# Kernel optimization log

Measured on AMD Instinct MI355X. Metric: run time of the kernel, lower is better.

Reference implementation:

```python
import jax, jax.numpy as jnp
import numpy as np
from jax import lax

NSAMPLE = 1024
SEM_NUM = 20


def weighted_fps(xyz, w, nsample):
    # xyz: [B,N,3], w: [B,N] -> idx [B,nsample] int32
    # Iterative weighted furthest point sampling: start at index 0, keep the
    # min squared distance to the selected set, pick argmax(min_dist * weight).
    B, N, _ = xyz.shape
    barange = jnp.arange(B)

    def step(carry, _):
        min_d, last = carry                      # [B,N], [B]
        lp = xyz[barange, last]                  # [B,3] last selected points
        d = jnp.sum((xyz - lp[:, None, :]) ** 2, axis=-1)  # [B,N]
        min_d = jnp.minimum(min_d, d)
        nxt = jnp.argmax(min_d * w, axis=1).astype(jnp.int32)
        return (min_d, nxt), nxt

    init = (jnp.full((B, N), 1e10, xyz.dtype), jnp.zeros((B,), jnp.int32))
    _, rest = lax.scan(step, init, None, length=nsample - 1)   # [nsample-1, B]
    idx = jnp.concatenate([jnp.zeros((1, B), jnp.int32), rest], axis=0)
    return idx.T                                               # [B, nsample]


def setup_inputs() -> dict:
    key = jax.random.key(0)
    k1, k2, k3 = jax.random.split(key, 3)
    B, N, C = 16, 16384, 128
    xyz = jax.random.normal(k1, (B, N, 3), dtype=jnp.float32)
    seg_feature = jax.random.normal(k2, (B, C, N), dtype=jnp.float32)
    seg_label = jax.random.randint(k3, (B, N), 0, SEM_NUM, dtype=jnp.int32)
    return {"xyz": xyz, "seg_feature": seg_feature, "seg_label": seg_label}


def reference(xyz, seg_feature, seg_label):
    # class frequency weights: count[b,c] = #points of class c in cloud b
    counts = jnp.sum(jax.nn.one_hot(seg_label, SEM_NUM, dtype=jnp.float32), axis=1)  # [B,SEM]
    seg_weights = jnp.take_along_axis(counts, seg_label, axis=1)                     # [B,N]
    idx = weighted_fps(lax.stop_gradient(xyz), seg_weights, NSAMPLE)                 # [B,S]
    sampled_xyz = jnp.take_along_axis(xyz, idx[:, :, None], axis=1)                  # [B,S,3]
    sample_seg_feature = jnp.take_along_axis(seg_feature, idx[:, None, :], axis=2)   # [B,C,S]
    sample_seg_label = jnp.take_along_axis(seg_label, idx, axis=1)                   # [B,S]
    return sampled_xyz, sample_seg_feature, sample_seg_label
```

## Files before the change

### kernel.cpp

```cpp
#include <hip/hip_runtime.h>


#define FPS_B   16
#define FPS_N   16384
#define FPS_C   128
#define FPS_S   1024
#define FPS_SEM 20
#define FPS_T   1024
#define FPS_PPT 16

typedef unsigned long long ull;

template <int CTRL>
__device__ __forceinline__ float dpp_movf(float v) {
  return __uint_as_float(__builtin_amdgcn_update_dpp(
      __float_as_uint(v), __float_as_uint(v), CTRL, 0xF, 0xF, true));
}

__global__ __launch_bounds__(FPS_T)
__attribute__((amdgpu_waves_per_eu(4, 4)))
void wfps_kernel(
    const float* __restrict__ xyz,
    const int*   __restrict__ label,
    int*         __restrict__ idx_out)
{
  const int b = blockIdx.x;
  const int t = threadIdx.x;
  const int lane = t & 63;
  const int wave = t >> 6;

  __shared__ int counts[FPS_SEM];
  __shared__ float wvmax[16];
  __shared__ int widx[FPS_S];

  if (t < FPS_SEM) counts[t] = 0;
  widx[t] = 0x7FFFFFFF;
  __syncthreads();

  const int* lab = label + b * FPS_N;
  int mylab[FPS_PPT];
#pragma unroll
  for (int k = 0; k < FPS_PPT; ++k) {
    mylab[k] = lab[t + k * FPS_T];
    atomicAdd(&counts[mylab[k]], 1);
  }
  __syncthreads();

  const float* xb = xyz + b * FPS_N * 3;
  float px[FPS_PPT], py[FPS_PPT], pz[FPS_PPT], w[FPS_PPT], mind[FPS_PPT];
#pragma unroll
  for (int k = 0; k < FPS_PPT; ++k) {
    int n = t + k * FPS_T;
    px[k] = xb[n * 3 + 0];
    py[k] = xb[n * 3 + 1];
    pz[k] = xb[n * 3 + 2];
    w[k] = (float)counts[mylab[k]];
    mind[k] = 1e10f;
    asm("" : "+v"(px[k]), "+v"(py[k]), "+v"(pz[k]), "+v"(w[k]));
  }

  if (t == 0) idx_out[b * FPS_S] = 0;
  float lx = xb[0], ly = xb[1], lz = xb[2];

#pragma unroll 2
  for (int s = 1; s < FPS_S; ++s) {
    float bs = -1.0f;
#pragma unroll
    for (int k = 0; k < FPS_PPT; k += 2) {
      float dx0 = __fsub_rn(px[k], lx);
      float dy0 = __fsub_rn(py[k], ly);
      float dz0 = __fsub_rn(pz[k], lz);
      float d0  = __fadd_rn(__fadd_rn(__fmul_rn(dx0, dx0), __fmul_rn(dy0, dy0)),
                            __fmul_rn(dz0, dz0));
      float m0 = fminf(mind[k], d0);
      mind[k] = m0;
      float sc0 = __fmul_rn(m0, w[k]);

      float dx1 = __fsub_rn(px[k + 1], lx);
      float dy1 = __fsub_rn(py[k + 1], ly);
      float dz1 = __fsub_rn(pz[k + 1], lz);
      float d1  = __fadd_rn(__fadd_rn(__fmul_rn(dx1, dx1), __fmul_rn(dy1, dy1)),
                            __fmul_rn(dz1, dz1));
      float m1 = fminf(mind[k + 1], d1);
      mind[k + 1] = m1;
      float sc1 = __fmul_rn(m1, w[k + 1]);

      bs = fmaxf(fmaxf(bs, sc0), sc1);
    }

    float m = bs;
    m = fmaxf(m, dpp_movf<0xB1>(m));
    m = fmaxf(m, dpp_movf<0x4E>(m));
    m = fmaxf(m, dpp_movf<0x141>(m));
    m = fmaxf(m, dpp_movf<0x140>(m));
    m = fmaxf(m, dpp_movf<0x142>(m));
    m = fmaxf(m, dpp_movf<0x143>(m));

    if (lane == 63) wvmax[wave] = m;
    __syncthreads();

    float M = wvmax[lane & 15];
    M = fmaxf(M, dpp_movf<0xB1>(M));
    M = fmaxf(M, dpp_movf<0x4E>(M));
    M = fmaxf(M, dpp_movf<0x141>(M));
    M = fmaxf(M, dpp_movf<0x140>(M));

    unsigned Mbits = __float_as_uint(M);
    if (__float_as_uint(bs) == Mbits) {
      int bk = 0;
#pragma unroll
      for (int k = FPS_PPT - 1; k >= 0; --k)
        if (__float_as_uint(__fmul_rn(mind[k], w[k])) == Mbits) bk = k;
      atomicMin(&widx[s], t + (bk << 10));
    }
    __syncthreads();

    int cur = __builtin_amdgcn_readfirstlane(widx[s]);
    if (t == 0) idx_out[b * FPS_S + s] = cur;

    const float* q = xb + 3 * cur;
    lx = q[0]; ly = q[1]; lz = q[2];
  }
}

__global__ void gather_kernel(
    const float* __restrict__ xyz,
    const float* __restrict__ feat,
    const int*   __restrict__ label,
    const int*   __restrict__ idx,
    float*       __restrict__ out)
{
  const long long FEAT = (long long)FPS_B * FPS_C * FPS_S;
  const int XYZN = FPS_B * FPS_S * 3;
  const int LABN = FPS_B * FPS_S;
  long long i = (long long)blockIdx.x * blockDim.x + threadIdx.x;

  if (i < FEAT) {
    int s = (int)(i & (FPS_S - 1));
    int c = (int)((i >> 10) & (FPS_C - 1));
    int b = (int)(i >> 17);
    int n = idx[b * FPS_S + s];
    out[XYZN + i] = feat[((long long)(b * FPS_C + c)) * FPS_N + n];
  } else if (i < FEAT + XYZN) {
    int j = (int)(i - FEAT);
    int d = j % 3;
    int sb = j / 3;
    int s = sb & (FPS_S - 1);
    int b = sb >> 10;
    int n = idx[b * FPS_S + s];
    out[j] = xyz[((long long)b * FPS_N + n) * 3 + d];
  } else if (i < FEAT + XYZN + LABN) {
    int j = (int)(i - FEAT - XYZN);
    int s = j & (FPS_S - 1);
    int b = j >> 10;
    int n = idx[b * FPS_S + s];
    out[FEAT + XYZN + j] = (float)label[b * FPS_N + n];
  }
}

extern "C" void kernel_launch(void* const* d_in, const int* in_sizes, int n_in,
                              void* d_out, int out_size, void* d_ws, size_t ws_size,
                              hipStream_t stream) {
  const float* xyz   = (const float*)d_in[0];
  const float* feat  = (const float*)d_in[1];
  const int*   label = (const int*)d_in[2];
  float* out = (float*)d_out;
  int*   idx = (int*)d_ws;

  wfps_kernel<<<FPS_B, FPS_T, 0, stream>>>(xyz, label, idx);

  const long long total = (long long)FPS_B * FPS_C * FPS_S
                        + (long long)FPS_B * FPS_S * 3
                        + (long long)FPS_B * FPS_S;
  gather_kernel<<<(int)((total + 255) / 256), 256, 0, stream>>>(
      xyz, feat, label, idx, out);
}
```

Before: 1.520 ms.

## Replace per-step workgroup barriers with LDS flag spin-waits in weighted FPS

The two __syncthreads per sampling step are replaced by per-step LDS slots. Each wave publishes its max into a row initialised to a sentinel and polls until all 16 slots are filled. A per-step done counter, also polled, signals that the atomicMin on the selected index has finished. Using a fresh row for every step avoids reset races. The intent is to cut barrier latency in the 1023-step serial loop. The cost is busy polling that competes for issue slots with waves still computing, reliance on LDS ordering without explicit fences, and a bounded spin that could silently produce a wrong index on timeout. The unroll-2 pragma is also removed.

Measured after the change: 1.799 ms. 18.4% more time.

```diff
diff --git a/kernel.cpp b/kernel.cpp
--- a/kernel.cpp
+++ b/kernel.cpp
@@ -30,10 +30,17 @@
   const int wave = t >> 6;
 
   __shared__ int counts[FPS_SEM];
-  __shared__ float wvmax[16];
+  __shared__ unsigned wvs[FPS_S][16];
+  __shared__ unsigned done[FPS_S];
   __shared__ int widx[FPS_S];
 
   if (t < FPS_SEM) counts[t] = 0;
+  {
+    uint4 f = make_uint4(0xFFFFFFFFu, 0xFFFFFFFFu, 0xFFFFFFFFu, 0xFFFFFFFFu);
+    uint4* r = (uint4*)&wvs[t][0];
+    r[0] = f; r[1] = f; r[2] = f; r[3] = f;
+  }
+  done[t] = 0u;
   widx[t] = 0x7FFFFFFF;
   __syncthreads();
 
@@ -62,7 +69,6 @@
   if (t == 0) idx_out[b * FPS_S] = 0;
   float lx = xb[0], ly = xb[1], lz = xb[2];
 
-#pragma unroll 2
   for (int s = 1; s < FPS_S; ++s) {
     float bs = -1.0f;
 #pragma unroll
@@ -96,16 +102,22 @@
     m = fmaxf(m, dpp_movf<0x142>(m));
     m = fmaxf(m, dpp_movf<0x143>(m));
 
-    if (lane == 63) wvmax[wave] = m;
-    __syncthreads();
+    if (lane == 63)
+      *((volatile unsigned*)&wvs[s][wave]) = __float_as_uint(m);
 
-    float M = wvmax[lane & 15];
+    volatile unsigned* rowA = (volatile unsigned*)&wvs[s][0];
+    unsigned va;
+    int g1 = 0;
+    do { va = rowA[lane & 15]; }
+    while (__ballot(va != 0xFFFFFFFFu) != ~0ull && ++g1 < 65536);
+
+    float M = __uint_as_float(va);
     M = fmaxf(M, dpp_movf<0xB1>(M));
     M = fmaxf(M, dpp_movf<0x4E>(M));
     M = fmaxf(M, dpp_movf<0x141>(M));
     M = fmaxf(M, dpp_movf<0x140>(M));
+    unsigned Mbits = __float_as_uint(M);
 
-    unsigned Mbits = __float_as_uint(M);
     if (__float_as_uint(bs) == Mbits) {
       int bk = 0;
 #pragma unroll
@@ -113,9 +125,17 @@
         if (__float_as_uint(__fmul_rn(mind[k], w[k])) == Mbits) bk = k;
       atomicMin(&widx[s], t + (bk << 10));
     }
-    __syncthreads();
+    if (lane == 63) atomicAdd(&done[s], 1u);
 
-    int cur = __builtin_amdgcn_readfirstlane(widx[s]);
+    volatile unsigned* dp = (volatile unsigned*)&done[s];
+    unsigned dv;
+    int g2 = 0;
+    do { dv = *dp; }
+    while (dv != 16u && ++g2 < 65536);
+
+    int cur = *((volatile int*)&widx[s]);
+    cur = __builtin_amdgcn_readfirstlane(cur) & (FPS_N - 1);
+
     if (t == 0) idx_out[b * FPS_S + s] = cur;
 
     const float* q = xb + 3 * cur;
```
